# Kernel optimization log

Measured on AMD Instinct MI355X. Metric: run time of the kernel, lower is better.

The kernel has to match this reference:

```python
import jax, jax.numpy as jnp
import numpy as np

B, T, D = 32, 512, 64   # batch, timesteps, latent dim
H, S = 64, 4096         # hidden_size, state_dim
EPS = 1e-6              # flax LayerNorm default epsilon


def _glorot(k, shape):
    lim = np.sqrt(6.0 / (shape[0] + shape[1])).astype(np.float32)
    return jax.random.uniform(k, shape, jnp.float32, -lim, lim)


def setup_inputs() -> dict:
    key = jax.random.key(0)
    ks = jax.random.split(key, 7)
    # gate order in the fused 4H axis: i, f, g, o ; flax inits f-gate bias to 1
    bh = jnp.concatenate([jnp.zeros((H,)), jnp.ones((H,)), jnp.zeros((2 * H,))]).astype(jnp.float32)
    return {
        "enc_outputs": jax.random.normal(ks[0], (B, T, D), jnp.float32),
        "Wx": _glorot(ks[1], (D, 4 * H)),   # input->gates, no bias (flax dense_i)
        "Wh": _glorot(ks[2], (H, 4 * H)),   # hidden->gates
        "bh": bh,
        "W1": _glorot(ks[3], (H, 2 * H)), "b1": jnp.zeros((2 * H,), jnp.float32),
        "g1": jnp.ones((2 * H,), jnp.float32), "be1": jnp.zeros((2 * H,), jnp.float32),
        "W2": _glorot(ks[4], (2 * H, 2 * H)), "b2": jnp.zeros((2 * H,), jnp.float32),
        "g2": jnp.ones((2 * H,), jnp.float32), "be2": jnp.zeros((2 * H,), jnp.float32),
        "Wo": _glorot(ks[5], (2 * H, S)), "bo": jnp.zeros((S,), jnp.float32),
    }


def _layernorm(x, g, b):
    m = x.mean(-1, keepdims=True)
    v = ((x - m) ** 2).mean(-1, keepdims=True)
    return (x - m) * jax.lax.rsqrt(v + EPS) * g + b


def _lstm(enc, Wx, Wh, bh):
    # precompute all input projections in one big GEMM: [B,T,4H]
    xg = jnp.einsum('btd,dg->btg', enc, Wx)

    def step(carry, x_t):
        c, h = carry
        z = x_t + h @ Wh + bh              # [B,4H]
        i, f, g, o = jnp.split(z, 4, axis=-1)
        c = jax.nn.sigmoid(f) * c + jax.nn.sigmoid(i) * jnp.tanh(g)
        h = jax.nn.sigmoid(o) * jnp.tanh(c)
        return (c, h), h

    b = enc.shape[0]
    init = (jnp.zeros((b, H), enc.dtype), jnp.zeros((b, H), enc.dtype))
    _, hs = jax.lax.scan(step, init, xg.swapaxes(0, 1))  # hs: [T,B,H]
    return hs.swapaxes(0, 1)                              # [B,T,H]


def reference(enc_outputs, Wx, Wh, bh, W1, b1, g1, be1, W2, b2, g2, be2, Wo, bo):
    b, t, _ = enc_outputs.shape
    dec = _lstm(enc_outputs, Wx, Wh, bh)            # [B,T,H]
    flat = dec.reshape(b * t, H)
    h = jax.nn.gelu(_layernorm(flat @ W1 + b1, g1, be1))   # flax gelu: tanh approx
    # dropout deterministic (train=False) -> identity
    h = jax.nn.gelu(_layernorm(h @ W2 + b2, g2, be2))
    out = h @ Wo + bo                                # [B*T,S]
    return out.reshape(b, t, S)
```

## Files before the change

kernel.cpp:

```cpp
#include <hip/hip_runtime.h>
#include <hip/hip_bf16.h>

#define T_ 512

typedef __attribute__((ext_vector_type(8))) short short8;
typedef __attribute__((ext_vector_type(4))) float f32x4;

__device__ __forceinline__ float fast_rcp(float x){ return __builtin_amdgcn_rcpf(x); }
__device__ __forceinline__ float sigmoid_f(float x){
  x = fminf(fmaxf(x, -30.f), 30.f);
  return fast_rcp(1.f + __expf(-x));
}
__device__ __forceinline__ float tanh_f(float x){
  x = fminf(fmaxf(x, -15.f), 15.f);
  return fmaf(2.f, fast_rcp(1.f + __expf(-2.f*x)), -1.f);
}
__device__ __forceinline__ float gelu_f(float x){
  float u = 0.7978845608028654f*(x + 0.044715f*x*x*x);
  return 0.5f*x*(1.f + tanh_f(u));
}

__global__ __launch_bounds__(256) void k_xg(const float* __restrict__ enc,
                                            const float* __restrict__ Wx,
                                            const float* __restrict__ bh,
                                            float* __restrict__ xg)
{
  __shared__ __align__(16) float es[64*64];
  int j = threadIdx.x;
  int g = blockIdx.x;
  const float* encg = enc + (size_t)g*64*64;
  for (int idx = j; idx < 64*64; idx += 256) es[idx] = encg[idx];
  float wx[64];
#pragma unroll
  for (int k = 0; k < 64; ++k) wx[k] = Wx[k*256 + j];
  float bj = bh[j];
  __syncthreads();
  float* xo = xg + (size_t)g*64*256;
  for (int r = 0; r < 64; ++r){
    const float4* e4 = (const float4*)(es + r*64);
    float z0 = bj, z1 = 0.f, z2 = 0.f, z3 = 0.f;
#pragma unroll
    for (int k4 = 0; k4 < 16; ++k4){
      float4 v = e4[k4];
      z0 = fmaf(v.x, wx[4*k4+0], z0);
      z1 = fmaf(v.y, wx[4*k4+1], z1);
      z2 = fmaf(v.z, wx[4*k4+2], z2);
      z3 = fmaf(v.w, wx[4*k4+3], z3);
    }
    xo[r*256 + j] = (z0+z1)+(z2+z3);
  }
}

__global__ __launch_bounds__(256) void k_lstm(const float* __restrict__ xg,
                                              const float* __restrict__ Wh,
                                              float* __restrict__ hs)
{
  __shared__ __align__(16) float hb[2][64];
  int tid = threadIdx.x;
  int w = tid >> 6, l = tid & 63;
  int m = w*16 + (l & 15);
  int g = l >> 4;
  int j = g*64 + m;
  int b = blockIdx.x;
  float wh[64];
#pragma unroll
  for (int k = 0; k < 64; ++k) wh[k] = Wh[k*256 + j];
  bool upd = (l < 16);
  float c = 0.f;
  if (tid < 64) hb[0][tid] = 0.f;
  const float* xr = xg + (size_t)b*T_*256;
  float* ho = hs + (size_t)b*T_*64;
  float xnext = xr[j];
  __syncthreads();
  for (int t = 0; t < T_; ++t){
    const float4* h4 = (const float4*)hb[t & 1];
    float z0 = xnext, z1 = 0.f, z2 = 0.f, z3 = 0.f;
    if (t+1 < T_) xnext = xr[(size_t)(t+1)*256 + j];
#pragma unroll
    for (int k4 = 0; k4 < 16; ++k4){
      float4 v = h4[k4];
      z0 = fmaf(v.x, wh[4*k4+0], z0);
      z1 = fmaf(v.y, wh[4*k4+1], z1);
      z2 = fmaf(v.z, wh[4*k4+2], z2);
      z3 = fmaf(v.w, wh[4*k4+3], z3);
    }
    float z = (z0+z1)+(z2+z3);
    float zB = __shfl_xor(z, 16);
    float zC = __shfl_xor(z, 32);
    float zD = __shfl_xor(z, 48);
    if (upd){
      c = sigmoid_f(zB)*c + sigmoid_f(z)*tanh_f(zC);
      float h = sigmoid_f(zD)*tanh_f(c);
      hb[(t+1) & 1][m] = h;
      ho[(size_t)t*64 + m] = h;
    }
    __syncthreads();
  }
}

__global__ __launch_bounds__(256) void k_mlp(const float* __restrict__ hs,
    const float* __restrict__ W1, const float* __restrict__ b1,
    const float* __restrict__ g1, const float* __restrict__ be1,
    const float* __restrict__ W2, const float* __restrict__ b2,
    const float* __restrict__ g2, const float* __restrict__ be2,
    __hip_bfloat16* __restrict__ h2g)
{
  __shared__ __align__(16) float xs[2][64];
  __shared__ __align__(16) float vs[2][128];
  __shared__ float red[2][2][2];
  int tid = threadIdx.x;
  int jj = tid & 127, rg = tid >> 7;
  int lane = tid & 63;
  int whalf = (tid >> 6) & 1;
  float w1c[64], w2c[128];
#pragma unroll
  for (int k = 0; k < 64; ++k) w1c[k] = W1[k*128 + jj];
#pragma unroll
  for (int k = 0; k < 128; ++k) w2c[k] = W2[k*128 + jj];
  float b1j = b1[jj], g1j = g1[jj], be1j = be1[jj];
  float b2j = b2[jj], g2j = g2[jj], be2j = be2[jj];
  int base = blockIdx.x * 64;
  for (int p = 0; p < 32; ++p){
    int r = base + p*2 + rg;
    if (whalf == 0) xs[rg][lane] = hs[(size_t)r*64 + lane];
    __syncthreads();
    float a0 = b1j, a1 = 0.f;
    const float4* x4 = (const float4*)xs[rg];
#pragma unroll
    for (int k4 = 0; k4 < 16; ++k4){
      float4 v = x4[k4];
      a0 = fmaf(v.x, w1c[4*k4+0], a0);
      a1 = fmaf(v.y, w1c[4*k4+1], a1);
      a0 = fmaf(v.z, w1c[4*k4+2], a0);
      a1 = fmaf(v.w, w1c[4*k4+3], a1);
    }
    float a = a0 + a1;
    float s1 = a, s2 = a*a;
#pragma unroll
    for (int off = 32; off > 0; off >>= 1){
      s1 += __shfl_xor(s1, off, 64);
      s2 += __shfl_xor(s2, off, 64);
    }
    if (lane == 0){ red[rg][whalf][0] = s1; red[rg][whalf][1] = s2; }
    __syncthreads();
    s1 = red[rg][0][0] + red[rg][1][0];
    s2 = red[rg][0][1] + red[rg][1][1];
    float mean = s1*(1.f/128.f);
    float var  = s2*(1.f/128.f) - mean*mean;
    float rstd = rsqrtf(var + 1e-6f);
    float y = gelu_f((a - mean)*rstd*g1j + be1j);
    vs[rg][jj] = y;
    __syncthreads();
    float c0 = b2j, c1 = 0.f;
    const float4* v4 = (const float4*)vs[rg];
#pragma unroll
    for (int k4 = 0; k4 < 32; ++k4){
      float4 v = v4[k4];
      c0 = fmaf(v.x, w2c[4*k4+0], c0);
      c1 = fmaf(v.y, w2c[4*k4+1], c1);
      c0 = fmaf(v.z, w2c[4*k4+2], c0);
      c1 = fmaf(v.w, w2c[4*k4+3], c1);
    }
    float cc = c0 + c1;
    float t1 = cc, t2 = cc*cc;
#pragma unroll
    for (int off = 32; off > 0; off >>= 1){
      t1 += __shfl_xor(t1, off, 64);
      t2 += __shfl_xor(t2, off, 64);
    }
    if (lane == 0){ red[rg][whalf][0] = t1; red[rg][whalf][1] = t2; }
    __syncthreads();
    t1 = red[rg][0][0] + red[rg][1][0];
    t2 = red[rg][0][1] + red[rg][1][1];
    mean = t1*(1.f/128.f);
    var  = t2*(1.f/128.f) - mean*mean;
    rstd = rsqrtf(var + 1e-6f);
    float z = gelu_f((cc - mean)*rstd*g2j + be2j);
    h2g[(size_t)r*128 + jj] = __float2bfloat16(z);
  }
}

__global__ __launch_bounds__(256) void k_wot(const float* __restrict__ Wo,
                                             __hip_bfloat16* __restrict__ WoT)
{
  __shared__ __hip_bfloat16 tl[64][130];
  int tid = threadIdx.x;
  int n0 = blockIdx.x * 64;
  for (int idx = tid; idx < 64*128; idx += 256){
    int k = idx >> 6, nl = idx & 63;
    tl[nl][k] = __float2bfloat16(Wo[(size_t)k*4096 + n0 + nl]);
  }
  __syncthreads();
  for (int idx = tid; idx < 64*128; idx += 256){
    int nl = idx >> 7, k = idx & 127;
    WoT[(size_t)(n0 + nl)*128 + k] = tl[nl][k];
  }
}

__global__ __launch_bounds__(256) void k_out(const __hip_bfloat16* __restrict__ h2g,
                                             const __hip_bfloat16* __restrict__ WoT,
                                             const float* __restrict__ bo,
                                             float* __restrict__ out)
{
  int bid = blockIdx.x;
  int Mb = bid >> 6, Nb = bid & 63;
  int tid = threadIdx.x;
  int w = tid >> 6, l = tid & 63;
  int wn = w >> 1, wm = w & 1;
  int n0 = Nb*64 + wn*32, m0 = Mb*64 + wm*32;
  int lr = l & 15, lk = (l >> 4)*8;
  f32x4 acc00 = {0.f,0.f,0.f,0.f}, acc01 = {0.f,0.f,0.f,0.f};
  f32x4 acc10 = {0.f,0.f,0.f,0.f}, acc11 = {0.f,0.f,0.f,0.f};
  const short* A  = (const short*)WoT;
  const short* Bp = (const short*)h2g;
#pragma unroll
  for (int kk = 0; kk < 4; ++kk){
    int ko = kk*32 + lk;
    short8 a0 = *(const short8*)(A  + (size_t)(n0      + lr)*128 + ko);
    short8 a1 = *(const short8*)(A  + (size_t)(n0 + 16 + lr)*128 + ko);
    short8 b0 = *(const short8*)(Bp + (size_t)(m0      + lr)*128 + ko);
    short8 b1 = *(const short8*)(Bp + (size_t)(m0 + 16 + lr)*128 + ko);
    acc00 = __builtin_amdgcn_mfma_f32_16x16x32_bf16(a0, b0, acc00, 0, 0, 0);
    acc01 = __builtin_amdgcn_mfma_f32_16x16x32_bf16(a0, b1, acc01, 0, 0, 0);
    acc10 = __builtin_amdgcn_mfma_f32_16x16x32_bf16(a1, b0, acc10, 0, 0, 0);
    acc11 = __builtin_amdgcn_mfma_f32_16x16x32_bf16(a1, b1, acc11, 0, 0, 0);
  }
  int nb_ = (l >> 4)*4;
  f32x4 bia0 = *(const f32x4*)(bo + n0 + nb_);
  f32x4 bia1 = *(const f32x4*)(bo + n0 + 16 + nb_);
  size_t row0 = (size_t)(m0 + lr)*4096;
  size_t row1 = (size_t)(m0 + 16 + lr)*4096;
  __builtin_nontemporal_store(acc00 + bia0, (f32x4*)(out + row0 + n0 + nb_));
  __builtin_nontemporal_store(acc10 + bia1, (f32x4*)(out + row0 + n0 + 16 + nb_));
  __builtin_nontemporal_store(acc01 + bia0, (f32x4*)(out + row1 + n0 + nb_));
  __builtin_nontemporal_store(acc11 + bia1, (f32x4*)(out + row1 + n0 + 16 + nb_));
}

extern "C" void kernel_launch(void* const* d_in, const int* in_sizes, int n_in,
                              void* d_out, int out_size, void* d_ws, size_t ws_size,
                              hipStream_t stream)
{
  const float* enc = (const float*)d_in[0];
  const float* Wx  = (const float*)d_in[1];
  const float* Wh  = (const float*)d_in[2];
  const float* bh  = (const float*)d_in[3];
  const float* W1  = (const float*)d_in[4];
  const float* b1  = (const float*)d_in[5];
  const float* g1  = (const float*)d_in[6];
  const float* be1 = (const float*)d_in[7];
  const float* W2  = (const float*)d_in[8];
  const float* b2  = (const float*)d_in[9];
  const float* g2  = (const float*)d_in[10];
  const float* be2 = (const float*)d_in[11];
  const float* Wo  = (const float*)d_in[12];
  const float* bo  = (const float*)d_in[13];
  float* out = (float*)d_out;

  const size_t xg_bytes = (size_t)16384*256*4;
  const size_t hs_bytes = (size_t)16384*64*4;
  const size_t h2_bytes = (size_t)16384*128*2;
  const size_t wt_bytes = (size_t)4096*128*2;
  char* ws = (char*)d_ws;
  float *xg, *hs; __hip_bfloat16 *h2g, *WoT;
  if (ws_size >= xg_bytes + hs_bytes + h2_bytes + wt_bytes){
    xg  = (float*)ws;
    hs  = (float*)(ws + xg_bytes);
    h2g = (__hip_bfloat16*)(ws + xg_bytes + hs_bytes);
    WoT = (__hip_bfloat16*)(ws + xg_bytes + hs_bytes + h2_bytes);
  } else {
    xg  = (float*)d_out;
    hs  = (float*)((char*)d_out + xg_bytes);
    h2g = (__hip_bfloat16*)ws;
    WoT = (__hip_bfloat16*)(ws + h2_bytes);
  }

  k_xg  <<<256,   256, 0, stream>>>(enc, Wx, bh, xg);
  k_wot <<<64,    256, 0, stream>>>(Wo, WoT);
  k_lstm<<<32,    256, 0, stream>>>(xg, Wh, hs);
  k_mlp <<<256,   256, 0, stream>>>(hs, W1, b1, g1, be1, W2, b2, g2, be2, h2g);
  k_out <<<16384, 256, 0, stream>>>(h2g, WoT, bo, out);
}
```

Measured before the change: 511.3 us.

## Enlarge output GEMM tiles, prefetch LSTM inputs deeper, drop activation clamps

The output GEMM kernel now gives each wave a 64x64 tile built from a 4x4 grid of MFMAs over a 128x128 block tile. Fewer blocks are launched, and each loaded fragment is reused across four MFMAs. The LSTM recurrence is unrolled by four, with x-gate inputs prefetched four steps ahead to hide global load latency on the serial path. The clamps in sigmoid and tanh are removed to shorten the per-step dependency chain, at the risk of inf/NaN for extreme inputs (exp overflow gives rcp(inf)=0, which is still fine).

Result: faster. 471.4 us (-7.8%).

```diff
diff --git a/kernel.cpp b/kernel.cpp
--- a/kernel.cpp
+++ b/kernel.cpp
@@ -8,11 +8,9 @@
 
 __device__ __forceinline__ float fast_rcp(float x){ return __builtin_amdgcn_rcpf(x); }
 __device__ __forceinline__ float sigmoid_f(float x){
-  x = fminf(fmaxf(x, -30.f), 30.f);
   return fast_rcp(1.f + __expf(-x));
 }
 __device__ __forceinline__ float tanh_f(float x){
-  x = fminf(fmaxf(x, -15.f), 15.f);
   return fmaf(2.f, fast_rcp(1.f + __expf(-2.f*x)), -1.f);
 }
 __device__ __forceinline__ float gelu_f(float x){
@@ -70,32 +68,45 @@
   if (tid < 64) hb[0][tid] = 0.f;
   const float* xr = xg + (size_t)b*T_*256;
   float* ho = hs + (size_t)b*T_*64;
-  float xnext = xr[j];
+  float xn0 = xr[j];
+  float xn1 = xr[256 + j];
+  float xn2 = xr[512 + j];
+  float xn3 = xr[768 + j];
   __syncthreads();
-  for (int t = 0; t < T_; ++t){
-    const float4* h4 = (const float4*)hb[t & 1];
-    float z0 = xnext, z1 = 0.f, z2 = 0.f, z3 = 0.f;
-    if (t+1 < T_) xnext = xr[(size_t)(t+1)*256 + j];
-#pragma unroll
-    for (int k4 = 0; k4 < 16; ++k4){
-      float4 v = h4[k4];
-      z0 = fmaf(v.x, wh[4*k4+0], z0);
-      z1 = fmaf(v.y, wh[4*k4+1], z1);
-      z2 = fmaf(v.z, wh[4*k4+2], z2);
-      z3 = fmaf(v.w, wh[4*k4+3], z3);
-    }
-    float z = (z0+z1)+(z2+z3);
-    float zB = __shfl_xor(z, 16);
-    float zC = __shfl_xor(z, 32);
-    float zD = __shfl_xor(z, 48);
-    if (upd){
-      c = sigmoid_f(zB)*c + sigmoid_f(z)*tanh_f(zC);
-      float h = sigmoid_f(zD)*tanh_f(c);
-      hb[(t+1) & 1][m] = h;
-      ho[(size_t)t*64 + m] = h;
-    }
-    __syncthreads();
-  }
+
+#define LSTM_STEP(tt, xn)                                                     \
+  {                                                                           \
+    const float4* h4 = (const float4*)hb[(tt) & 1];                           \
+    float z0 = (xn), z1 = 0.f, z2 = 0.f, z3 = 0.f;                            \
+    if ((tt) + 4 < T_) (xn) = xr[(size_t)((tt) + 4)*256 + j];                 \
+    _Pragma("unroll")                                                         \
+    for (int k4 = 0; k4 < 16; ++k4){                                          \
+      float4 v = h4[k4];                                                      \
+      z0 = fmaf(v.x, wh[4*k4+0], z0);                                         \
+      z1 = fmaf(v.y, wh[4*k4+1], z1);                                         \
+      z2 = fmaf(v.z, wh[4*k4+2], z2);                                         \
+      z3 = fmaf(v.w, wh[4*k4+3], z3);                                         \
+    }                                                                         \
+    float z = (z0+z1)+(z2+z3);                                                \
+    float zB = __shfl_xor(z, 16);                        \
+    float zC = __shfl_xor(z, 32);                        \
+    float zD = __shfl_xor(z, 48);                        \
+    if (upd){                                                                 \
+      c = sigmoid_f(zB)*c + sigmoid_f(z)*tanh_f(zC);                          \
+      float h = sigmoid_f(zD)*tanh_f(c);                                      \
+      hb[((tt)+1) & 1][m] = h;                                                \
+      ho[(size_t)(tt)*64 + m] = h;                                            \
+    }                                                                         \
+    __syncthreads();                                                          \
+  }
+
+  for (int t = 0; t < T_; t += 4){
+    LSTM_STEP(t,   xn0);
+    LSTM_STEP(t+1, xn1);
+    LSTM_STEP(t+2, xn2);
+    LSTM_STEP(t+3, xn3);
+  }
+#undef LSTM_STEP
 }
 
 __global__ __launch_bounds__(256) void k_mlp(const float* __restrict__ hs,
@@ -203,37 +214,39 @@
                                              float* __restrict__ out)
 {
   int bid = blockIdx.x;
-  int Mb = bid >> 6, Nb = bid & 63;
+  int Mb = bid >> 5, Nb = bid & 31;
   int tid = threadIdx.x;
   int w = tid >> 6, l = tid & 63;
-  int wn = w >> 1, wm = w & 1;
-  int n0 = Nb*64 + wn*32, m0 = Mb*64 + wm*32;
+  int wm = w >> 1, wn = w & 1;
+  int m0 = Mb*128 + wm*64, n0 = Nb*128 + wn*64;
   int lr = l & 15, lk = (l >> 4)*8;
-  f32x4 acc00 = {0.f,0.f,0.f,0.f}, acc01 = {0.f,0.f,0.f,0.f};
-  f32x4 acc10 = {0.f,0.f,0.f,0.f}, acc11 = {0.f,0.f,0.f,0.f};
+  f32x4 acc[4][4] = {};
   const short* A  = (const short*)WoT;
   const short* Bp = (const short*)h2g;
 #pragma unroll
   for (int kk = 0; kk < 4; ++kk){
     int ko = kk*32 + lk;
-    short8 a0 = *(const short8*)(A  + (size_t)(n0      + lr)*128 + ko);
-    short8 a1 = *(const short8*)(A  + (size_t)(n0 + 16 + lr)*128 + ko);
-    short8 b0 = *(const short8*)(Bp + (size_t)(m0      + lr)*128 + ko);
-    short8 b1 = *(const short8*)(Bp + (size_t)(m0 + 16 + lr)*128 + ko);
-    acc00 = __builtin_amdgcn_mfma_f32_16x16x32_bf16(a0, b0, acc00, 0, 0, 0);
-    acc01 = __builtin_amdgcn_mfma_f32_16x16x32_bf16(a0, b1, acc01, 0, 0, 0);
-    acc10 = __builtin_amdgcn_mfma_f32_16x16x32_bf16(a1, b0, acc10, 0, 0, 0);
-    acc11 = __builtin_amdgcn_mfma_f32_16x16x32_bf16(a1, b1, acc11, 0, 0, 0);
+    short8 av[4], bv[4];
+#pragma unroll
+    for (int i = 0; i < 4; ++i) av[i] = *(const short8*)(A  + (size_t)(n0 + i*16 + lr)*128 + ko);
+#pragma unroll
+    for (int i = 0; i < 4; ++i) bv[i] = *(const short8*)(Bp + (size_t)(m0 + i*16 + lr)*128 + ko);
+#pragma unroll
+    for (int fm = 0; fm < 4; ++fm)
+#pragma unroll
+      for (int fn = 0; fn < 4; ++fn)
+        acc[fm][fn] = __builtin_amdgcn_mfma_f32_16x16x32_bf16(av[fn], bv[fm], acc[fm][fn], 0, 0, 0);
   }
   int nb_ = (l >> 4)*4;
-  f32x4 bia0 = *(const f32x4*)(bo + n0 + nb_);
-  f32x4 bia1 = *(const f32x4*)(bo + n0 + 16 + nb_);
-  size_t row0 = (size_t)(m0 + lr)*4096;
-  size_t row1 = (size_t)(m0 + 16 + lr)*4096;
-  __builtin_nontemporal_store(acc00 + bia0, (f32x4*)(out + row0 + n0 + nb_));
-  __builtin_nontemporal_store(acc10 + bia1, (f32x4*)(out + row0 + n0 + 16 + nb_));
-  __builtin_nontemporal_store(acc01 + bia0, (f32x4*)(out + row1 + n0 + nb_));
-  __builtin_nontemporal_store(acc11 + bia1, (f32x4*)(out + row1 + n0 + 16 + nb_));
+#pragma unroll
+  for (int fn = 0; fn < 4; ++fn){
+    f32x4 bia = *(const f32x4*)(bo + n0 + fn*16 + nb_);
+#pragma unroll
+    for (int fm = 0; fm < 4; ++fm){
+      size_t row = (size_t)(m0 + fm*16 + lr)*4096;
+      __builtin_nontemporal_store(acc[fm][fn] + bia, (f32x4*)(out + row + n0 + fn*16 + nb_));
+    }
+  }
 }
 
 extern "C" void kernel_launch(void* const* d_in, const int* in_sizes, int n_in,
@@ -274,9 +287,9 @@
     WoT = (__hip_bfloat16*)(ws + h2_bytes);
   }
 
-  k_xg  <<<256,   256, 0, stream>>>(enc, Wx, bh, xg);
-  k_wot <<<64,    256, 0, stream>>>(Wo, WoT);
-  k_lstm<<<32,    256, 0, stream>>>(xg, Wh, hs);
-  k_mlp <<<256,   256, 0, stream>>>(hs, W1, b1, g1, be1, W2, b2, g2, be2, h2g);
-  k_out <<<16384, 256, 0, stream>>>(h2g, WoT, bo, out);
-}
+  k_xg  <<<256,  256, 0, stream>>>(enc, Wx, bh, xg);
+  k_wot <<<64,   256, 0, stream>>>(Wo, WoT);
+  k_lstm<<<32,   256, 0, stream>>>(xg, Wh, hs);
+  k_mlp <<<256,  256, 0, stream>>>(hs, W1, b1, g1, be1, W2, b2, g2, be2, h2g);
+  k_out <<<4096, 256, 0, stream>>>(h2g, WoT, bo, out);
+}
```
